# Kernel optimization log

Measured on AMD Instinct MI355X. Metric: run time of the kernel, lower is better.

## Reference

```python
import jax, jax.numpy as jnp
import numpy as np

FLOOR = float(np.finfo(np.float32).eps)   # torch.finfo(float32).eps
CEIL = float(np.finfo(np.float32).max)    # torch.finfo(float32).max


def window_sum(x, window_size):
    # Sum over a (window_size x window_size) sliding window, VALID padding.
    # Equivalent to the separable depthwise conv-of-ones in the torch code.
    return jax.lax.reduce_window(
        x, 0.0, jax.lax.add,
        window_dimensions=(1, 1, window_size, window_size),
        window_strides=(1, 1, 1, 1),
        padding='VALID')


def setup_inputs() -> dict:
    key = jax.random.key(0)
    k1, k2, k3 = jax.random.split(key, 3)
    B, C, H1, W1 = 16, 32, 256, 256
    H2 = W2 = 64
    feat_1 = jax.random.normal(k1, (B, C, H1, W1), dtype=jnp.float32)
    feat_2 = jax.random.normal(k2, (B, C, H2, W2), dtype=jnp.float32)
    # xcorr is the full cross-correlation map: (H1+H2-1, W1+W2-1)
    xcorr = jax.random.normal(k3, (B, C, H1 + H2 - 1, W1 + W2 - 1), dtype=jnp.float32)
    return {"feat_1": feat_1, "feat_2": feat_2, "xcorr": xcorr}


def reference(feat_1, feat_2, xcorr):
    # normalize_by_window == True branch (windowed NCC normalization)
    B, C, H1, W1 = feat_1.shape
    _, _, H2, W2 = feat_2.shape
    template_size = H2
    pad = template_size - 1
    opt_padded = jnp.pad(feat_1, ((0, 0), (0, 0), (pad, pad), (pad, pad)))
    sar_volume = float(H2 * W2)

    winsum = window_sum(opt_padded, template_size)            # (B,C,H1+H2-1,W1+W2-1)
    winsum2 = window_sum(opt_padded ** 2, template_size)

    f2_mean = feat_2.mean(axis=(2, 3), keepdims=True)          # (B,C,1,1)
    numerator = xcorr - winsum * f2_mean
    winsum2_corr = winsum2 - winsum ** 2 / sar_volume
    sar_ssd = ((feat_2 - f2_mean) ** 2).sum(axis=(2, 3), keepdims=True)

    denom = jnp.sqrt(jnp.clip(winsum2_corr * sar_ssd, 0.0, None))
    numerator_clipped = jnp.clip(numerator, FLOOR, CEIL)
    denom_clipped = jnp.clip(denom, FLOOR, CEIL)
    mask = denom > FLOOR
    return jnp.where(mask, numerator_clipped / denom_clipped, jnp.zeros_like(xcorr))
```

## Files before the change

kernel.cpp:

```cpp
#include <hip/hip_runtime.h>
#include <math.h>

#define H1 256
#define W1 256
#define HO 319
#define WO 319
#define SEG 8
#define ROWS_PER 40

__device__ __forceinline__ float up0(float x, int d, int lane) {
  float s = __shfl_up(x, (unsigned)d, 64);
  return (lane >= d) ? s : 0.0f;
}
__device__ __forceinline__ float dn0(float x, int d, int lane) {
  float s = __shfl_down(x, (unsigned)d, 64);
  return (lane + d <= 63) ? s : 0.0f;
}

__device__ __forceinline__ void win7(float a0, float a1, float a2, float a3,
                                     int lane, float wi[4], float wt[4]) {
  float L0 = a0, L1 = L0 + a1, L2 = L1 + a2, L3 = L2 + a3;
  float sf2 = a3, sf1 = sf2 + a2, sf0 = sf1 + a1;
  float b1 = L3 + up0(L3, 1, lane);
  float b2 = b1 + up0(b1, 2, lane);
  float b3 = b2 + up0(b2, 4, lane);
  float M = up0(b3, 1, lane) + up0(b2, 9, lane) + up0(b1, 13, lane) + up0(L3, 15, lane);
  float c1 = L3 + dn0(L3, 1, lane);
  float c2 = c1 + dn0(c1, 2, lane);
  float c3 = c2 + dn0(c2, 4, lane);
  float c4 = c3 + dn0(c3, 8, lane);
  float T49 = dn0(c4, 49, lane);
  float g0 = up0(sf0, 16, lane), g1 = up0(sf1, 16, lane), g2 = up0(sf2, 16, lane);
  float h0 = dn0(sf0, 48, lane), h1 = dn0(sf1, 48, lane), h2 = dn0(sf2, 48, lane);
  wi[0] = g0 + M + L0;  wi[1] = g1 + M + L1;  wi[2] = g2 + M + L2;  wi[3] = M + L3;
  wt[0] = h0 + T49;     wt[1] = h1 + T49;     wt[2] = h2 + T49;     wt[3] = T49;
}

__device__ __forceinline__ float out_val(float ws, float ws2, float xc,
                                         float mean, float ssd) {
  const float FLOOR_  = 1.1920928955078125e-07f;
  const float FLOOR2_ = FLOOR_ * FLOOR_;
  float num  = xc - ws * mean;
  float w2c  = ws2 - ws * ws * (1.0f / 4096.0f);
  float t    = fmaxf(w2c * ssd, 0.0f);
  float numc = fmaxf(num, FLOOR_);
  return (t > FLOOR2_) ? (numc * __frsqrt_rn(t)) : 0.0f;
}

__global__ __launch_bounds__(256)
void ncc_norm_kernel(const float* __restrict__ feat1,
                     const float* __restrict__ feat2,
                     const float* __restrict__ xcorr,
                     float* __restrict__ out) {
  const int tid  = threadIdx.x;
  const int lane = tid & 63;
  const int wv   = tid >> 6;
  const int bc   = blockIdx.y;
  const int seg  = blockIdx.x * 4 + wv;

  const float* f1 = feat1 + (size_t)bc * (H1 * W1);
  const float* f2 = feat2 + (size_t)bc * 4096;

  float sum = 0.0f, sumsq = 0.0f;
  #pragma unroll
  for (int r = 0; r < 16; ++r) {
    float4 q = *(const float4*)(f2 + r * 256 + 4 * lane);
    sum   += (q.x + q.y) + (q.z + q.w);
    sumsq += (q.x * q.x + q.y * q.y) + (q.z * q.z + q.w * q.w);
  }
  #pragma unroll
  for (int d = 1; d < 64; d <<= 1) {
    sum   += __shfl_xor(sum,   d, 64);
    sumsq += __shfl_xor(sumsq, d, 64);
  }
  float mean = sum * (1.0f / 4096.0f);
  float ssd  = sumsq - sum * mean;

  const int y0 = seg * ROWS_PER;
  const int y1 = min(HO, y0 + ROWS_PER);
  const int x4 = 4 * lane;

  double v0 = 0, v1 = 0, v2 = 0, v3 = 0;
  double q0 = 0, q1 = 0, q2 = 0, q3 = 0;
  for (int r = max(0, y0 - 64); r < min(y0, H1); ++r) {
    float4 t = *(const float4*)(f1 + r * W1 + x4);
    v0 += t.x; q0 += (double)t.x * t.x;
    v1 += t.y; q1 += (double)t.y * t.y;
    v2 += t.z; q2 += (double)t.z * t.z;
    v3 += t.w; q3 += (double)t.w * t.w;
  }

  for (int y = y0; y < y1; ++y) {
    if (y < H1) {
      float4 t = *(const float4*)(f1 + y * W1 + x4);
      v0 += t.x; q0 += (double)t.x * t.x;
      v1 += t.y; q1 += (double)t.y * t.y;
      v2 += t.z; q2 += (double)t.z * t.z;
      v3 += t.w; q3 += (double)t.w * t.w;
    }
    int yl = y - 64;
    if (yl >= 0) {
      float4 t = *(const float4*)(f1 + yl * W1 + x4);
      v0 -= t.x; q0 -= (double)t.x * t.x;
      v1 -= t.y; q1 -= (double)t.y * t.y;
      v2 -= t.z; q2 -= (double)t.z * t.z;
      v3 -= t.w; q3 -= (double)t.w * t.w;
    }

    float w0 = (float)v0, w1 = (float)v1, w2 = (float)v2, w3 = (float)v3;
    float u0 = (float)q0, u1 = (float)q1, u2 = (float)q2, u3 = (float)q3;

    float wsI[4], wsT[4], sqI[4], sqT[4];
    win7(w0, w1, w2, w3, lane, wsI, wsT);
    win7(u0, u1, u2, u3, lane, sqI, sqT);

    const int rowbase = (bc * HO + y) * WO;
    const float* xr = xcorr + rowbase;
    float*       orw = out  + rowbase;

    #pragma unroll
    for (int j = 0; j < 4; ++j) {
      float xc = xr[x4 + j];
      orw[x4 + j] = out_val(wsI[j], sqI[j], xc, mean, ssd);
    }
    if (lane < 16) {
      #pragma unroll
      for (int j = 0; j < 4; ++j) {
        int xo = 256 + x4 + j;
        if (xo < WO) {
          float xc = xr[xo];
          orw[xo] = out_val(wsT[j], sqT[j], xc, mean, ssd);
        }
      }
    }
  }
}

extern "C" void kernel_launch(void* const* d_in, const int* in_sizes, int n_in,
                              void* d_out, int out_size, void* d_ws, size_t ws_size,
                              hipStream_t stream) {
  const float* feat1 = (const float*)d_in[0];
  const float* feat2 = (const float*)d_in[1];
  const float* xcorr = (const float*)d_in[2];
  float* out = (float*)d_out;

  dim3 grid(SEG / 4, 512);
  ncc_norm_kernel<<<grid, 256, 0, stream>>>(feat1, feat2, xcorr, out);
}
```

Before: 554.5 us.

## Split rows finer, remap blocks per XCD, prefetch rows, use nontemporal xcorr/out

Rows are split into 16 segments of 20 instead of 8 of 40, which doubles the number of blocks, and the launch bounds now request 8 blocks per CU. A 1D grid remaps block IDs so that all blocks of one batch-channel land on the same XCD, aiming at L2 reuse of feat1 and feat2. Feature rows for the next iteration are software-prefetched, and xcorr loads are issued early so they overlap the shuffle work. Loads and stores on the streaming xcorr and out data use nontemporal hints. The cost is more redundant warm-up row accumulation per segment and more register pressure.

```diff
diff --git a/kernel.cpp b/kernel.cpp
--- a/kernel.cpp
+++ b/kernel.cpp
@@ -5,8 +5,8 @@
 #define W1 256
 #define HO 319
 #define WO 319
-#define SEG 8
-#define ROWS_PER 40
+#define SEG 16
+#define ROWS_PER 20
 
 __device__ __forceinline__ float up0(float x, int d, int lane) {
   float s = __shfl_up(x, (unsigned)d, 64);
@@ -47,7 +47,7 @@
   return (t > FLOOR2_) ? (numc * __frsqrt_rn(t)) : 0.0f;
 }
 
-__global__ __launch_bounds__(256)
+__global__ __launch_bounds__(256, 8)
 void ncc_norm_kernel(const float* __restrict__ feat1,
                      const float* __restrict__ feat2,
                      const float* __restrict__ xcorr,
@@ -55,8 +55,12 @@
   const int tid  = threadIdx.x;
   const int lane = tid & 63;
   const int wv   = tid >> 6;
-  const int bc   = blockIdx.y;
-  const int seg  = blockIdx.x * 4 + wv;
+
+  const int d   = blockIdx.x;
+  const int xcd = d & 7;
+  const int i   = d >> 3;
+  const int bc  = xcd * 64 + (i >> 2);
+  const int seg = (i & 3) * 4 + wv;
 
   const float* f1 = feat1 + (size_t)bc * (H1 * W1);
   const float* f2 = feat2 + (size_t)bc * 4096;
@@ -69,9 +73,9 @@
     sumsq += (q.x * q.x + q.y * q.y) + (q.z * q.z + q.w * q.w);
   }
   #pragma unroll
-  for (int d = 1; d < 64; d <<= 1) {
-    sum   += __shfl_xor(sum,   d, 64);
-    sumsq += __shfl_xor(sumsq, d, 64);
+  for (int dd = 1; dd < 64; dd <<= 1) {
+    sum   += __shfl_xor(sum,   dd, 64);
+    sumsq += __shfl_xor(sumsq, dd, 64);
   }
   float mean = sum * (1.0f / 4096.0f);
   float ssd  = sumsq - sum * mean;
@@ -90,21 +94,45 @@
     v3 += t.w; q3 += (double)t.w * t.w;
   }
 
+  float4 tE, tL;
+  if (y0 < H1)  tE = *(const float4*)(f1 + y0 * W1 + x4);
+  if (y0 >= 64) tL = *(const float4*)(f1 + (y0 - 64) * W1 + x4);
+
   for (int y = y0; y < y1; ++y) {
+    const int rowbase = (bc * HO + y) * WO;
+    const float* xr  = xcorr + rowbase;
+    float*       orw = out   + rowbase;
+
+    float xi[4];
+    #pragma unroll
+    for (int j = 0; j < 4; ++j) xi[j] = __builtin_nontemporal_load(xr + x4 + j);
+    float xt[4] = {0.0f, 0.0f, 0.0f, 0.0f};
+    if (lane < 16) {
+      xt[0] = __builtin_nontemporal_load(xr + 256 + x4 + 0);
+      xt[1] = __builtin_nontemporal_load(xr + 256 + x4 + 1);
+      xt[2] = __builtin_nontemporal_load(xr + 256 + x4 + 2);
+      if (lane < 15) xt[3] = __builtin_nontemporal_load(xr + 256 + x4 + 3);
+    }
+
     if (y < H1) {
-      float4 t = *(const float4*)(f1 + y * W1 + x4);
-      v0 += t.x; q0 += (double)t.x * t.x;
-      v1 += t.y; q1 += (double)t.y * t.y;
-      v2 += t.z; q2 += (double)t.z * t.z;
-      v3 += t.w; q3 += (double)t.w * t.w;
+      v0 += tE.x; q0 += (double)tE.x * tE.x;
+      v1 += tE.y; q1 += (double)tE.y * tE.y;
+      v2 += tE.z; q2 += (double)tE.z * tE.z;
+      v3 += tE.w; q3 += (double)tE.w * tE.w;
     }
-    int yl = y - 64;
-    if (yl >= 0) {
-      float4 t = *(const float4*)(f1 + yl * W1 + x4);
-      v0 -= t.x; q0 -= (double)t.x * t.x;
-      v1 -= t.y; q1 -= (double)t.y * t.y;
-      v2 -= t.z; q2 -= (double)t.z * t.z;
-      v3 -= t.w; q3 -= (double)t.w * t.w;
+    if (y >= 64) {
+      v0 -= tL.x; q0 -= (double)tL.x * tL.x;
+      v1 -= tL.y; q1 -= (double)tL.y * tL.y;
+      v2 -= tL.z; q2 -= (double)tL.z * tL.z;
+      v3 -= tL.w; q3 -= (double)tL.w * tL.w;
+    }
+
+    {
+      int yn = y + 1;
+      if (yn < y1) {
+        if (yn < H1)  tE = *(const float4*)(f1 + yn * W1 + x4);
+        if (yn >= 64) tL = *(const float4*)(f1 + (yn - 64) * W1 + x4);
+      }
     }
 
     float w0 = (float)v0, w1 = (float)v1, w2 = (float)v2, w3 = (float)v3;
@@ -114,24 +142,16 @@
     win7(w0, w1, w2, w3, lane, wsI, wsT);
     win7(u0, u1, u2, u3, lane, sqI, sqT);
 
-    const int rowbase = (bc * HO + y) * WO;
-    const float* xr = xcorr + rowbase;
-    float*       orw = out  + rowbase;
-
     #pragma unroll
-    for (int j = 0; j < 4; ++j) {
-      float xc = xr[x4 + j];
-      orw[x4 + j] = out_val(wsI[j], sqI[j], xc, mean, ssd);
-    }
+    for (int j = 0; j < 4; ++j)
+      __builtin_nontemporal_store(out_val(wsI[j], sqI[j], xi[j], mean, ssd),
+                                  orw + x4 + j);
     if (lane < 16) {
-      #pragma unroll
-      for (int j = 0; j < 4; ++j) {
-        int xo = 256 + x4 + j;
-        if (xo < WO) {
-          float xc = xr[xo];
-          orw[xo] = out_val(wsT[j], sqT[j], xc, mean, ssd);
-        }
-      }
+      __builtin_nontemporal_store(out_val(wsT[0], sqT[0], xt[0], mean, ssd), orw + 256 + x4 + 0);
+      __builtin_nontemporal_store(out_val(wsT[1], sqT[1], xt[1], mean, ssd), orw + 256 + x4 + 1);
+      __builtin_nontemporal_store(out_val(wsT[2], sqT[2], xt[2], mean, ssd), orw + 256 + x4 + 2);
+      if (lane < 15)
+        __builtin_nontemporal_store(out_val(wsT[3], sqT[3], xt[3], mean, ssd), orw + 256 + x4 + 3);
     }
   }
 }
@@ -144,6 +164,6 @@
   const float* xcorr = (const float*)d_in[2];
   float* out = (float*)d_out;
 
-  dim3 grid(SEG / 4, 512);
+  dim3 grid(512 * SEG / 4);
   ncc_norm_kernel<<<grid, 256, 0, stream>>>(feat1, feat2, xcorr, out);
 }
```

New measurement: 634.2 us. +14.4%, slower.
